# Kernel optimization log

Hardware: AMD Instinct MI355X
Metric: run time of the kernel (lower is better)

Reference implementation:

```python
import jax, jax.numpy as jnp
import numpy as np

EPS = 1e-6

def setup_inputs() -> dict:
    key = jax.random.key(0)
    k1, k2, k3 = jax.random.split(key, 3)
    B, N, D = 2048, 50000, 1024
    x = jax.random.normal(k1, (B, D), dtype=jnp.float32)
    W = jax.random.normal(k2, (D, D), dtype=jnp.float32) * (1.0 / np.sqrt(D))
    target_embeddings = jax.random.normal(k3, (N, D), dtype=jnp.float32)
    return {"x": x, "W": W, "target_embeddings": target_embeddings}

def reference(x, W, target_embeddings):
    # Linear(dim, dim, bias=False): y = x @ W.T  (W stored [out, in] as in torch)
    t = x @ W.T                                   # (B, D)
    # Fused cosine similarity: normalize once, single GEMM against the bank.
    t_norm = jnp.linalg.norm(t, axis=-1)          # (B,)
    e_norm = jnp.linalg.norm(target_embeddings, axis=-1)  # (N,)
    dots = t @ target_embeddings.T                # (B, N)
    denom = jnp.maximum(t_norm[:, None] * e_norm[None, :], EPS)
    return dots / denom                           # (B, N)
```

## Files before the change

kernel.cpp:

```cpp
#include <hip/hip_runtime.h>

typedef unsigned short u16;
typedef __attribute__((ext_vector_type(4))) float f32x4;
typedef __attribute__((ext_vector_type(4))) unsigned short u16x4;
typedef __attribute__((ext_vector_type(8))) unsigned short u16x8;
typedef __attribute__((ext_vector_type(8))) __bf16 bf16x8;

#define BM 128
#define BN 128
#define BK 32

__device__ __forceinline__ u16 f2bf(float f) {
  unsigned int u = __float_as_uint(f);
  u = (u + 0x7FFFu + ((u >> 16) & 1u)) >> 16;
  return (u16)u;
}
__device__ __forceinline__ float bf2f(u16 v) {
  return __uint_as_float(((unsigned int)v) << 16);
}

typedef const void __attribute__((address_space(1)))* gas1_t;
typedef void __attribute__((address_space(3)))* las3_t;
__device__ __forceinline__ void gload_lds16(const void* g, void* l) {
  __builtin_amdgcn_global_load_lds((gas1_t)g, (las3_t)l, 16, 0, 0);
}

__global__ __launch_bounds__(256) void conv_f32_bf16(const float* __restrict__ in,
                                                     u16* __restrict__ out, int n8) {
  int i = blockIdx.x * 256 + threadIdx.x;
  if (i >= n8) return;
  const f32x4* p = (const f32x4*)in + (size_t)i * 2;
  f32x4 a = p[0], b = p[1];
  u16x8 o;
  o[0]=f2bf(a[0]); o[1]=f2bf(a[1]); o[2]=f2bf(a[2]); o[3]=f2bf(a[3]);
  o[4]=f2bf(b[0]); o[5]=f2bf(b[1]); o[6]=f2bf(b[2]); o[7]=f2bf(b[3]);
  *((u16x8*)out + i) = o;
}

__global__ __launch_bounds__(256) void conv_rows_norm(const float* __restrict__ in,
                                                      u16* __restrict__ out,
                                                      float* __restrict__ inv_norm,
                                                      int nrows_in, int D) {
  const int row = blockIdx.x;
  const int tid = threadIdx.x;
  float ss = 0.0f;
  if (row < nrows_in) {
    for (int j = tid * 4; j < D; j += 1024) {
      f32x4 v = *((const f32x4*)(in + (size_t)row * D + j));
      u16x4 o; o[0]=f2bf(v[0]); o[1]=f2bf(v[1]); o[2]=f2bf(v[2]); o[3]=f2bf(v[3]);
      *((u16x4*)(out + (size_t)row * D + j)) = o;
      ss += v[0]*v[0] + v[1]*v[1] + v[2]*v[2] + v[3]*v[3];
    }
  } else {
    for (int j = tid * 4; j < D; j += 1024) {
      u16x4 o = (u16x4)0;
      *((u16x4*)(out + (size_t)row * D + j)) = o;
    }
  }
  for (int off = 32; off > 0; off >>= 1) ss += __shfl_down(ss, off, 64);
  __shared__ float red[4];
  if ((tid & 63) == 0) red[tid >> 6] = ss;
  __syncthreads();
  if (tid == 0) {
    float s = red[0] + red[1] + red[2] + red[3];
    inv_norm[row] = (row < nrows_in) ? (1.0f / sqrtf(s)) : 1.0f;
  }
}

__global__ __launch_bounds__(256) void rownorm_bf16(const u16* __restrict__ in,
                                                    float* __restrict__ inv_norm, int D) {
  const int row = blockIdx.x;
  const int tid = threadIdx.x;
  float ss = 0.0f;
  for (int j = tid * 4; j < D; j += 1024) {
    u16x4 v = *((const u16x4*)(in + (size_t)row * D + j));
    float f0 = bf2f(v[0]), f1 = bf2f(v[1]), f2 = bf2f(v[2]), f3 = bf2f(v[3]);
    ss += f0*f0 + f1*f1 + f2*f2 + f3*f3;
  }
  for (int off = 32; off > 0; off >>= 1) ss += __shfl_down(ss, off, 64);
  __shared__ float red[4];
  if ((tid & 63) == 0) red[tid >> 6] = ss;
  __syncthreads();
  if (tid == 0) inv_norm[row] = 1.0f / sqrtf(red[0] + red[1] + red[2] + red[3]);
}

template<bool SCALED>
__global__ __launch_bounds__(256)
void gemm_nt(const u16* __restrict__ A, const u16* __restrict__ Bm,
             float* __restrict__ Cf, u16* __restrict__ Cbf,
             const float* __restrict__ rinv, const float* __restrict__ cinv,
             int K, int Nt, int ldc)
{
  __shared__ u16 As[BM * BK];
  __shared__ u16 Bs[BN * BK];

  const int tid  = threadIdx.x;
  const int wave = tid >> 6;
  const int lane = tid & 63;
  const int wm = wave >> 1, wn = wave & 1;
  const int fl = lane & 15, fh = lane >> 4;
  const int tile_m = blockIdx.x * BM;
  const int tile_n = blockIdx.y * BN;

  const int srow = lane >> 2;
  const int scol = (lane & 3) * 8;

  const u16* Ag = A  + (size_t)(tile_m + wave * 32 + srow) * K + scol;
  const u16* Bg = Bm + (size_t)(tile_n + wave * 32 + srow) * K + scol;
  u16* AsB = &As[(wave * 32) * BK];
  u16* BsB = &Bs[(wave * 32) * BK];

  f32x4 acc[4][4] = {};

  for (int k0 = 0; k0 < K; k0 += BK) {
    __syncthreads();
    gload_lds16(Ag,           AsB);
    gload_lds16(Ag + 16 * K,  AsB + 16 * BK);
    gload_lds16(Bg,           BsB);
    gload_lds16(Bg + 16 * K,  BsB + 16 * BK);
    Ag += BK; Bg += BK;
    __syncthreads();

    bf16x8 av[4], bv[4];
#pragma unroll
    for (int mt = 0; mt < 4; ++mt)
      av[mt] = *((const bf16x8*)&As[(wm * 64 + mt * 16 + fl) * BK + fh * 8]);
#pragma unroll
    for (int nt = 0; nt < 4; ++nt)
      bv[nt] = *((const bf16x8*)&Bs[(wn * 64 + nt * 16 + fl) * BK + fh * 8]);
#pragma unroll
    for (int mt = 0; mt < 4; ++mt)
#pragma unroll
      for (int nt = 0; nt < 4; ++nt)
        acc[mt][nt] = __builtin_amdgcn_mfma_f32_16x16x32_bf16(av[mt], bv[nt], acc[mt][nt], 0, 0, 0);
  }

  if constexpr (SCALED) {
#pragma unroll
    for (int mt = 0; mt < 4; ++mt) {
      const int r0 = tile_m + wm * 64 + mt * 16 + fh * 4;
      const float t0 = rinv[r0], t1 = rinv[r0 + 1], t2 = rinv[r0 + 2], t3 = rinv[r0 + 3];
#pragma unroll
      for (int nt = 0; nt < 4; ++nt) {
        const int c = tile_n + wn * 64 + nt * 16 + fl;
        if (c < Nt) {
          const float ei = cinv[c];
          f32x4 v = acc[mt][nt];
          float* p = Cf + (size_t)r0 * ldc + c;
          p[0]                 = v[0] * t0 * ei;
          p[(size_t)ldc]       = v[1] * t1 * ei;
          p[(size_t)ldc * 2]   = v[2] * t2 * ei;
          p[(size_t)ldc * 3]   = v[3] * t3 * ei;
        }
      }
    }
  } else {
#pragma unroll
    for (int mt = 0; mt < 4; ++mt) {
      const int r0 = tile_m + wm * 64 + mt * 16 + fh * 4;
#pragma unroll
      for (int nt = 0; nt < 4; ++nt) {
        const int c = tile_n + wn * 64 + nt * 16 + fl;
        u16* p = Cbf + (size_t)r0 * ldc + c;
        f32x4 v = acc[mt][nt];
        p[0]               = f2bf(v[0]);
        p[(size_t)ldc]     = f2bf(v[1]);
        p[(size_t)ldc * 2] = f2bf(v[2]);
        p[(size_t)ldc * 3] = f2bf(v[3]);
      }
    }
  }
}

extern "C" void kernel_launch(void* const* d_in, const int* in_sizes, int n_in,
                              void* d_out, int out_size, void* d_ws, size_t ws_size,
                              hipStream_t stream) {
  const float* x = (const float*)d_in[0];
  const float* W = (const float*)d_in[1];
  const float* E = (const float*)d_in[2];
  float* out = (float*)d_out;

  const int Dm = 1024;
  const int B  = in_sizes[0] / Dm;
  const int N  = in_sizes[2] / Dm;
  const int Npad = ((N + BN - 1) / BN) * BN;

  char* ws = (char*)d_ws;
  u16* e_bf = (u16*)ws;
  size_t off = (size_t)Npad * Dm * sizeof(u16);
  u16* x_bf = (u16*)(ws + off); off += (size_t)B  * Dm * sizeof(u16);
  u16* w_bf = (u16*)(ws + off); off += (size_t)Dm * Dm * sizeof(u16);
  u16* t_bf = (u16*)(ws + off); off += (size_t)B  * Dm * sizeof(u16);
  float* e_inv = (float*)(ws + off); off += (size_t)Npad * sizeof(float);
  float* t_inv = (float*)(ws + off);

  conv_f32_bf16<<<(B * Dm / 8 + 255) / 256, 256, 0, stream>>>(x, x_bf, B * Dm / 8);
  conv_f32_bf16<<<(Dm * Dm / 8 + 255) / 256, 256, 0, stream>>>(W, w_bf, Dm * Dm / 8);
  conv_rows_norm<<<Npad, 256, 0, stream>>>(E, e_bf, e_inv, N, Dm);

  gemm_nt<false><<<dim3(B / BM, Dm / BN), 256, 0, stream>>>(
      x_bf, w_bf, nullptr, t_bf, nullptr, nullptr, Dm, Dm, Dm);
  rownorm_bf16<<<B, 256, 0, stream>>>(t_bf, t_inv, Dm);

  gemm_nt<true><<<dim3(B / BM, Npad / BN), 256, 0, stream>>>(
      t_bf, e_bf, out, nullptr, t_inv, e_inv, Dm, N, N);
}
```

Before: 878.5 us.

## Replace big similarity GEMM with 256x256 triple-buffered swizzled MFMA kernel

The large t·E^T GEMM gets its own kernel. It uses 256x256 tiles with 512 threads, triple-buffered LDS fed by direct global-to-LDS loads, and an XOR-swizzled LDS layout. Blocks are remapped across the grid to group tiles for L2 reuse, and s_setprio is raised around the MFMA blocks so loads overlap compute. Together these aim to raise arithmetic intensity and hide memory latency. In exchange it adds manual waitcnt/barrier bookkeeping and more register pressure, and it clamps B rows to stay in bounds.

```diff
diff --git a/kernel.cpp b/kernel.cpp
--- a/kernel.cpp
+++ b/kernel.cpp
@@ -23,6 +23,12 @@
 typedef void __attribute__((address_space(3)))* las3_t;
 __device__ __forceinline__ void gload_lds16(const void* g, void* l) {
   __builtin_amdgcn_global_load_lds((gas1_t)g, (las3_t)l, 16, 0, 0);
+}
+
+__device__ __forceinline__ void bar() {
+  asm volatile("" ::: "memory");
+  __builtin_amdgcn_s_barrier();
+  asm volatile("" ::: "memory");
 }
 
 __global__ __launch_bounds__(256) void conv_f32_bf16(const float* __restrict__ in,
@@ -84,12 +90,9 @@
   if (tid == 0) inv_norm[row] = 1.0f / sqrtf(red[0] + red[1] + red[2] + red[3]);
 }
 
-template<bool SCALED>
 __global__ __launch_bounds__(256)
-void gemm_nt(const u16* __restrict__ A, const u16* __restrict__ Bm,
-             float* __restrict__ Cf, u16* __restrict__ Cbf,
-             const float* __restrict__ rinv, const float* __restrict__ cinv,
-             int K, int Nt, int ldc)
+void gemm_nt_small(const u16* __restrict__ A, const u16* __restrict__ Bm,
+                   u16* __restrict__ Cbf, int K, int ldc)
 {
   __shared__ u16 As[BM * BK];
   __shared__ u16 Bs[BN * BK];
@@ -135,41 +138,145 @@
         acc[mt][nt] = __builtin_amdgcn_mfma_f32_16x16x32_bf16(av[mt], bv[nt], acc[mt][nt], 0, 0, 0);
   }
 
-  if constexpr (SCALED) {
-#pragma unroll
-    for (int mt = 0; mt < 4; ++mt) {
-      const int r0 = tile_m + wm * 64 + mt * 16 + fh * 4;
-      const float t0 = rinv[r0], t1 = rinv[r0 + 1], t2 = rinv[r0 + 2], t3 = rinv[r0 + 3];
-#pragma unroll
-      for (int nt = 0; nt < 4; ++nt) {
-        const int c = tile_n + wn * 64 + nt * 16 + fl;
-        if (c < Nt) {
-          const float ei = cinv[c];
-          f32x4 v = acc[mt][nt];
-          float* p = Cf + (size_t)r0 * ldc + c;
-          p[0]                 = v[0] * t0 * ei;
-          p[(size_t)ldc]       = v[1] * t1 * ei;
-          p[(size_t)ldc * 2]   = v[2] * t2 * ei;
-          p[(size_t)ldc * 3]   = v[3] * t3 * ei;
-        }
+#pragma unroll
+  for (int mt = 0; mt < 4; ++mt) {
+    const int r0 = tile_m + wm * 64 + mt * 16 + fh * 4;
+#pragma unroll
+    for (int nt = 0; nt < 4; ++nt) {
+      const int c = tile_n + wn * 64 + nt * 16 + fl;
+      u16* p = Cbf + (size_t)r0 * ldc + c;
+      f32x4 v = acc[mt][nt];
+      p[0]               = f2bf(v[0]);
+      p[(size_t)ldc]     = f2bf(v[1]);
+      p[(size_t)ldc * 2] = f2bf(v[2]);
+      p[(size_t)ldc * 3] = f2bf(v[3]);
+    }
+  }
+}
+
+#define GBM 256
+#define GBN 256
+#define GBK 32
+#define TELEM (GBM * GBK)
+#define NTM 8
+
+__global__ __launch_bounds__(512, 2)
+void gemm_nt_big(const u16* __restrict__ A, const u16* __restrict__ Bm,
+                 float* __restrict__ C,
+                 const float* __restrict__ rinv, const float* __restrict__ cinv,
+                 int K, int NB, int Nvalid, int ldc, int cpx)
+{
+  __shared__ u16 lds[3 * 2 * TELEM];
+
+  const int tt   = threadIdx.x;
+  const int wid  = tt >> 6;
+  const int lane = tt & 63;
+  const int wm = wid >> 2, wn = wid & 3;
+  const int fl = lane & 15, fh = lane >> 4;
+  const int flh = fl >> 1;
+  const int swz = ((((fl & 1) << 2) | fh) ^ flh) * 16;
+
+  const int gid = blockIdx.x;
+  const int tl  = (gid & 7) * cpx + (gid >> 3);
+  const int tile_m = (tl & (NTM - 1)) * GBM;
+  const int tile_n = (tl >> 3) * GBN;
+
+  const int sl   = (tt & 7) ^ ((tt >> 3) & 7);
+  const int srow = ((tt >> 3) << 1) + (sl >> 2);
+  const int scol = (sl & 3) * 8;
+
+  const u16* Ag0 = A + (size_t)(tile_m + srow) * K + scol;
+  const u16* Ag1 = Ag0 + (size_t)128 * K;
+  int br0 = tile_n + srow;       if (br0 > NB - 1) br0 = NB - 1;
+  int br1 = tile_n + srow + 128; if (br1 > NB - 1) br1 = NB - 1;
+  const u16* Bg0 = Bm + (size_t)br0 * K + scol;
+  const u16* Bg1 = Bm + (size_t)br1 * K + scol;
+
+#define STAGE_A(sbuf, ko) { char* d_ = (char*)(sbuf) + tt * 16; \
+    gload_lds16(Ag0 + (ko), d_); gload_lds16(Ag1 + (ko), d_ + 8192); }
+#define STAGE_B(sbuf, ko) { char* d_ = (char*)(sbuf) + tt * 16; \
+    gload_lds16(Bg0 + (ko), d_); gload_lds16(Bg1 + (ko), d_ + 8192); }
+
+  u16* A0 = lds;                 u16* B0 = lds + TELEM;
+  u16* A1 = lds + 2 * TELEM;     u16* B1 = lds + 3 * TELEM;
+  u16* A2 = lds + 4 * TELEM;     u16* B2 = lds + 5 * TELEM;
+
+  f32x4 acc[8][4] = {};
+
+  STAGE_A(A0, 0); STAGE_B(B0, 0);
+  STAGE_A(A1, GBK); STAGE_B(B1, GBK);
+  asm volatile("s_waitcnt vmcnt(4)" ::: "memory");
+  bar();
+
+  u16 *cA = A0, *cB = B0, *nA = A1, *nB = B1, *sA = A2, *sB = B2;
+  const int NT = K / GBK;
+  int ko = 2 * GBK;
+  const int komax = (NT - 1) * GBK;
+
+  for (int t = 0; t < NT; ++t) {
+    const char* pA = (const char*)cA;
+    const char* pB = (const char*)cB;
+    bf16x8 bv[4], av[4];
+
+#pragma unroll
+    for (int j = 0; j < 4; ++j)
+      bv[j] = *(const bf16x8*)(pB + ((((wn << 5) + j * 8 + flh) << 7) + swz));
+#pragma unroll
+    for (int i = 0; i < 4; ++i)
+      av[i] = *(const bf16x8*)(pA + ((((wm << 6) + i * 8 + flh) << 7) + swz));
+    STAGE_A(sA, ko);
+    bar();
+    __builtin_amdgcn_s_setprio(1);
+#pragma unroll
+    for (int i = 0; i < 4; ++i)
+#pragma unroll
+      for (int j = 0; j < 4; ++j)
+        acc[i][j] = __builtin_amdgcn_mfma_f32_16x16x32_bf16(av[i], bv[j], acc[i][j], 0, 0, 0);
+    __builtin_amdgcn_s_setprio(0);
+    bar();
+
+#pragma unroll
+    for (int i = 0; i < 4; ++i)
+      av[i] = *(const bf16x8*)(pA + ((((wm << 6) + (4 + i) * 8 + flh) << 7) + swz));
+    STAGE_B(sB, ko);
+    bar();
+    __builtin_amdgcn_s_setprio(1);
+#pragma unroll
+    for (int i = 0; i < 4; ++i)
+#pragma unroll
+      for (int j = 0; j < 4; ++j)
+        acc[4 + i][j] = __builtin_amdgcn_mfma_f32_16x16x32_bf16(av[i], bv[j], acc[4 + i][j], 0, 0, 0);
+    __builtin_amdgcn_s_setprio(0);
+
+    asm volatile("s_waitcnt lgkmcnt(0)" ::: "memory");
+    asm volatile("s_waitcnt vmcnt(4)" ::: "memory");
+    bar();
+
+    u16 *tA_ = cA, *tB_ = cB;
+    cA = nA; cB = nB; nA = sA; nB = sB; sA = tA_; sB = tB_;
+    ko += GBK; if (ko > komax) ko = komax;
+  }
+
+#pragma unroll
+  for (int mt = 0; mt < 8; ++mt) {
+    const int r0 = tile_m + wm * 128 + mt * 16 + fh * 4;
+    const float t0 = rinv[r0], t1 = rinv[r0 + 1], t2 = rinv[r0 + 2], t3 = rinv[r0 + 3];
+#pragma unroll
+    for (int nt = 0; nt < 4; ++nt) {
+      const int c = tile_n + wn * 64 + nt * 16 + fl;
+      if (c < Nvalid) {
+        const float ei = cinv[c];
+        f32x4 v = acc[mt][nt];
+        float* p = C + (size_t)r0 * ldc + c;
+        p[0]               = v[0] * t0 * ei;
+        p[(size_t)ldc]     = v[1] * t1 * ei;
+        p[(size_t)ldc * 2] = v[2] * t2 * ei;
+        p[(size_t)ldc * 3] = v[3] * t3 * ei;
       }
     }
-  } else {
-#pragma unroll
-    for (int mt = 0; mt < 4; ++mt) {
-      const int r0 = tile_m + wm * 64 + mt * 16 + fh * 4;
-#pragma unroll
-      for (int nt = 0; nt < 4; ++nt) {
-        const int c = tile_n + wn * 64 + nt * 16 + fl;
-        u16* p = Cbf + (size_t)r0 * ldc + c;
-        f32x4 v = acc[mt][nt];
-        p[0]               = f2bf(v[0]);
-        p[(size_t)ldc]     = f2bf(v[1]);
-        p[(size_t)ldc * 2] = f2bf(v[2]);
-        p[(size_t)ldc * 3] = f2bf(v[3]);
-      }
-    }
-  }
+  }
+#undef STAGE_A
+#undef STAGE_B
 }
 
 extern "C" void kernel_launch(void* const* d_in, const int* in_sizes, int n_in,
@@ -184,6 +291,8 @@
   const int B  = in_sizes[0] / Dm;
   const int N  = in_sizes[2] / Dm;
   const int Npad = ((N + BN - 1) / BN) * BN;
+  const int NTN = (N + GBN - 1) / GBN;
+  const int NWG = NTM * NTN;
 
   char* ws = (char*)d_ws;
   u16* e_bf = (u16*)ws;
@@ -198,10 +307,9 @@
   conv_f32_bf16<<<(Dm * Dm / 8 + 255) / 256, 256, 0, stream>>>(W, w_bf, Dm * Dm / 8);
   conv_rows_norm<<<Npad, 256, 0, stream>>>(E, e_bf, e_inv, N, Dm);
 
-  gemm_nt<false><<<dim3(B / BM, Dm / BN), 256, 0, stream>>>(
-      x_bf, w_bf, nullptr, t_bf, nullptr, nullptr, Dm, Dm, Dm);
+  gemm_nt_small<<<dim3(B / BM, Dm / BN), 256, 0, stream>>>(x_bf, w_bf, t_bf, Dm, Dm);
   rownorm_bf16<<<B, 256, 0, stream>>>(t_bf, t_inv, Dm);
 
-  gemm_nt<true><<<dim3(B / BM, Npad / BN), 256, 0, stream>>>(
-      t_bf, e_bf, out, nullptr, t_inv, e_inv, Dm, N, N);
-}
+  gemm_nt_big<<<NWG, 512, 0, stream>>>(t_bf, e_bf, out, t_inv, e_inv,
+                                       Dm, Npad, N, N, NWG / 8);
+}
```

After: 805.7 us. 1.09x faster.
